# Kernel tuning notes

Measured on AMD Instinct MI355X. Metric: run time of the kernel, lower is better.

Reference implementation:

```python
import jax, jax.numpy as jnp
import numpy as np

B, NP, NT = 16, 4096, 77
QD, CD, H, DH = 512, 768, 8, 64
INNER = H * DH


def setup_inputs() -> dict:
    key = jax.random.key(0)
    ks = jax.random.split(key, 8)
    s = 0.02
    return {
        "x": jax.random.normal(ks[0], (B, NP, QD), jnp.float32),
        "context": jax.random.normal(ks[1], (B, NT, CD), jnp.float32),
        "mask": jnp.ones((B, NP, NT), jnp.int32),
        "Wq": jax.random.normal(ks[2], (QD, INNER), jnp.float32) * s,
        "Wk": jax.random.normal(ks[3], (CD, INNER), jnp.float32) * s,
        "Wv": jax.random.normal(ks[4], (CD, INNER), jnp.float32) * s,
        "Wo": jax.random.normal(ks[5], (INNER, QD), jnp.float32) * s,
        "bo": jnp.zeros((QD,), jnp.float32),
    }


def reference(x, context, mask, Wq, Wk, Wv, Wo, bo):
    scale = 1.0 / jnp.sqrt(jnp.asarray(DH, x.dtype))
    # projections -> (B, H, N, DH)
    q = (x @ Wq).reshape(B, NP, H, DH).transpose(0, 2, 1, 3)
    k = (context @ Wk).reshape(B, NT, H, DH).transpose(0, 2, 1, 3)
    v = (context @ Wv).reshape(B, NT, H, DH).transpose(0, 2, 1, 3)
    # scores (B, H, NP, NT)
    attn = jnp.einsum("bhqd,bhkd->bhqk", q, k) * scale
    attn = jnp.where(mask[:, None, :, :] == 0, -jnp.inf, attn)
    attn = jax.nn.softmax(attn, axis=-1)
    out = jnp.einsum("bhqk,bhkd->bhqd", attn, v)
    out = out.transpose(0, 2, 1, 3).reshape(B, NP, INNER)
    return out @ Wo + bo
```

## Files before the change

kernel.cpp:

```cpp
#include <hip/hip_runtime.h>


typedef _Float16 half_t;
typedef _Float16 half8 __attribute__((ext_vector_type(8)));
typedef float f32x4 __attribute__((ext_vector_type(4)));
typedef unsigned int u32;

#define NB 16
#define NP 4096
#define NT 77
#define NTP 96
#define QD 512
#define CD 768
#define NH 8
#define DH 64
#define INNER 512
#define MKV (NB * NT)

__device__ __forceinline__ void stage16(const void* g, void* l) {
    __builtin_amdgcn_global_load_lds((const __attribute__((address_space(1))) u32*)g,
                                     (__attribute__((address_space(3))) u32*)l, 16, 0, 0);
}

__device__ __forceinline__ f32x4 mfma16(half8 a, half8 b, f32x4 c) {
    return __builtin_amdgcn_mfma_f32_16x16x32_f16(a, b, c, 0, 0, 0);
}

__global__ __launch_bounds__(256) void kTrans2(const float* __restrict__ in0,
                                               const float* __restrict__ in1,
                                               half_t* __restrict__ out0,
                                               half_t* __restrict__ out1,
                                               int K, int N) {
    const float* in = blockIdx.z ? in1 : in0;
    half_t* out = blockIdx.z ? out1 : out0;
    __shared__ float tile[32][33];
    int tx = threadIdx.x & 31, ty = threadIdx.x >> 5;
    int kb = blockIdx.y * 32, nb = blockIdx.x * 32;
    for (int r = ty; r < 32; r += 8)
        tile[r][tx] = in[(size_t)(kb + r) * N + nb + tx];
    __syncthreads();
    for (int r = ty; r < 32; r += 8)
        out[(size_t)(nb + r) * K + kb + tx] = (half_t)tile[tx][r];
}

__global__ __launch_bounds__(256) void kKVproj(const float* __restrict__ Ctx,
                                               const half_t* __restrict__ WkT,
                                               const half_t* __restrict__ WvT,
                                               half_t* __restrict__ Kp,
                                               half_t* __restrict__ VTp) {
    __shared__ alignas(16) half_t As[64 * 64];
    __shared__ alignas(16) half_t Bs[128 * 64];
    const int t = threadIdx.x, w = t >> 6, lane = t & 63;
    const int c0 = lane & 15, q4 = lane >> 4;
    const int rx = c0 & 7;
    const int m0 = blockIdx.y * 64;
    const int n0g = blockIdx.x * 128;
    const int z = n0g >= 512;
    const int n0 = n0g - z * 512;
    const half_t* WT = z ? WvT : WkT;

    f32x4 acc[4][2] = {};
    for (int k0 = 0; k0 < CD; k0 += 64) {
        for (int q = 0; q < 2; ++q) {
            int c = q * 256 + t;
            int row = c >> 3, ch = c & 7;
            int gr = m0 + row; if (gr > MKV - 1) gr = MKV - 1;
            const float* src = Ctx + (size_t)gr * CD + k0 + ch * 8;
            f32x4 f0 = *(const f32x4*)src;
            f32x4 f1 = *(const f32x4*)(src + 4);
            half8 hv;
            for (int e = 0; e < 4; ++e) { hv[e] = (half_t)f0[e]; hv[4 + e] = (half_t)f1[e]; }
            *(half8*)&As[row * 64 + ((ch ^ (row & 7)) * 8)] = hv;
        }
        for (int q = 0; q < 4; ++q) {
            int c = q * 256 + t;
            int row = c >> 3, k8 = c & 7;
            stage16(WT + (size_t)(n0 + row) * CD + k0 + (k8 ^ (row & 7)) * 8, &Bs[c * 8]);
        }
        __syncthreads();
        for (int ks = 0; ks < 2; ++ks) {
            int ch = ks * 4 + q4;
            int cx = (ch ^ rx) * 8;
            half8 a[4], b[2];
            for (int i = 0; i < 4; ++i)
                a[i] = *(const half8*)&As[(16 * i + c0) * 64 + cx];
            for (int j = 0; j < 2; ++j)
                b[j] = *(const half8*)&Bs[(w * 32 + 16 * j + c0) * 64 + cx];
            for (int i = 0; i < 4; ++i)
                for (int j = 0; j < 2; ++j)
                    acc[i][j] = mfma16(a[i], b[j], acc[i][j]);
        }
        __syncthreads();
    }
    for (int i = 0; i < 4; ++i)
        for (int j = 0; j < 2; ++j)
            for (int r = 0; r < 4; ++r) {
                int row = m0 + 16 * i + q4 * 4 + r;
                if (row >= MKV) continue;
                int col = n0 + w * 32 + 16 * j + c0;
                int b = row / NT, tt = row - b * NT;
                int h = col >> 6, d = col & 63;
                half_t v = (half_t)acc[i][j][r];
                if (!z) Kp[(((size_t)b * NH + h) * NTP + tt) * DH + d] = v;
                else    VTp[(((size_t)b * NH + h) * DH + d) * NTP + tt] = v;
            }
}

__global__ __launch_bounds__(256) void kQproj(const float* __restrict__ X,
                                              const half_t* __restrict__ WqT,
                                              half_t* __restrict__ Q) {
    __shared__ alignas(16) half_t As[128 * 64];
    __shared__ alignas(16) half_t Bs[128 * 64];
    const int t = threadIdx.x, w = t >> 6, lane = t & 63;
    const int c0 = lane & 15, q4 = lane >> 4;
    const int rx = c0 & 7;
    const int wm = w & 1, wn = w >> 1;
    const int bid = blockIdx.x;
    const int wid = (bid & 7) * 256 + (bid >> 3);
    const int m0 = (wid >> 2) * 128, n0 = (wid & 3) * 128;

    f32x4 acc[4][4] = {};
    for (int k0 = 0; k0 < QD; k0 += 64) {
        for (int q = 0; q < 4; ++q) {
            int c = q * 256 + t;
            int row = c >> 3, ch = c & 7;
            const float* src = X + (size_t)(m0 + row) * QD + k0 + ch * 8;
            f32x4 f0 = *(const f32x4*)src;
            f32x4 f1 = *(const f32x4*)(src + 4);
            half8 hv;
            for (int e = 0; e < 4; ++e) { hv[e] = (half_t)f0[e]; hv[4 + e] = (half_t)f1[e]; }
            *(half8*)&As[row * 64 + ((ch ^ (row & 7)) * 8)] = hv;
        }
        for (int q = 0; q < 4; ++q) {
            int c = q * 256 + t;
            int row = c >> 3, k8 = c & 7;
            stage16(WqT + (size_t)(n0 + row) * QD + k0 + (k8 ^ (row & 7)) * 8, &Bs[c * 8]);
        }
        __syncthreads();
        for (int ks = 0; ks < 2; ++ks) {
            int cx = ((ks * 4 + q4) ^ rx) * 8;
            half8 a[4];
            for (int i = 0; i < 4; ++i)
                a[i] = *(const half8*)&As[(wm * 64 + 16 * i + c0) * 64 + cx];
            for (int j = 0; j < 4; ++j) {
                half8 bv = *(const half8*)&Bs[(wn * 64 + 16 * j + c0) * 64 + cx];
                for (int i = 0; i < 4; ++i)
                    acc[i][j] = mfma16(a[i], bv, acc[i][j]);
            }
        }
        __syncthreads();
    }
    for (int i = 0; i < 4; ++i)
        for (int j = 0; j < 4; ++j)
            for (int r = 0; r < 4; ++r) {
                int row = m0 + wm * 64 + 16 * i + q4 * 4 + r;
                int col = n0 + wn * 64 + 16 * j + c0;
                Q[(size_t)row * INNER + col] = (half_t)acc[i][j][r];
            }
}

__global__ __launch_bounds__(256) void kAttn(half_t* __restrict__ Q,
                                             const half_t* __restrict__ Kp,
                                             const half_t* __restrict__ VTp,
                                             const int* __restrict__ mask) {
    __shared__ alignas(16) half_t Qs[128 * 104];
    __shared__ alignas(16) half_t Ks[NTP * 72];
    __shared__ alignas(16) half_t VTs[DH * 104];
    const int t = threadIdx.x, w = t >> 6, lane = t & 63;
    const int c0 = lane & 15, q4 = lane >> 4;
    const int qt = blockIdx.x, h = blockIdx.y, b = blockIdx.z;
    const int q0 = qt * 128;
    const size_t qbase = ((size_t)b * NP + q0) * INNER + h * DH;

    for (int q = 0; q < 4; ++q) {
        int c = q * 256 + t, m = c >> 3, k8 = (c & 7) * 8;
        *(uint4*)&Qs[m * 104 + k8] = *(const uint4*)(Q + qbase + (size_t)m * INNER + k8);
    }
    const half_t* Kh = Kp + ((size_t)b * NH + h) * NTP * DH;
    for (int q = 0; q < 3; ++q) {
        int c = q * 256 + t, r = c >> 3, k8 = (c & 7) * 8;
        *(uint4*)&Ks[r * 72 + k8] = *(const uint4*)(Kh + r * DH + k8);
    }
    const half_t* Vh = VTp + ((size_t)b * NH + h) * DH * NTP;
    for (int q = 0; q < 3; ++q) {
        int c = q * 256 + t, r = c / 12, t8 = (c % 12) * 8;
        *(uint4*)&VTs[r * 104 + t8] = *(const uint4*)(Vh + r * NTP + t8);
    }
    __syncthreads();

    const int r0 = w * 32;
    f32x4 sacc[2][6] = {};
    for (int ks = 0; ks < 2; ++ks) {
        half8 a0 = *(const half8*)&Qs[(r0 + c0) * 104 + ks * 32 + q4 * 8];
        half8 a1 = *(const half8*)&Qs[(r0 + 16 + c0) * 104 + ks * 32 + q4 * 8];
        for (int j = 0; j < 6; ++j) {
            half8 bv = *(const half8*)&Ks[(16 * j + c0) * 72 + ks * 32 + q4 * 8];
            sacc[0][j] = mfma16(a0, bv, sacc[0][j]);
            sacc[1][j] = mfma16(a1, bv, sacc[1][j]);
        }
    }

    for (int i = 0; i < 2; ++i)
        for (int r = 0; r < 4; ++r) {
            int qrow = r0 + 16 * i + q4 * 4 + r;
            const int* mrow = mask + ((size_t)b * NP + q0 + qrow) * NT;
            float sv[6];
            for (int j = 0; j < 6; ++j) {
                int tt = 16 * j + c0;
                float s = sacc[i][j][r] * 0.125f;
                bool valid = (tt < NT) && (mrow[tt < NT ? tt : NT - 1] != 0);
                sv[j] = valid ? s : -1e30f;
            }
            float mx = sv[0];
            for (int j = 1; j < 6; ++j) mx = fmaxf(mx, sv[j]);
            for (int d = 1; d < 16; d <<= 1) mx = fmaxf(mx, __shfl_xor(mx, d));
            float pv[6], sum = 0.f;
            for (int j = 0; j < 6; ++j) { pv[j] = __expf(sv[j] - mx); sum += pv[j]; }
            for (int d = 1; d < 16; d <<= 1) sum += __shfl_xor(sum, d);
            float inv = 1.0f / sum;
            for (int j = 0; j < 6; ++j)
                Qs[qrow * 104 + 16 * j + c0] = (half_t)(pv[j] * inv);
        }

    f32x4 oacc[2][4] = {};
    for (int ks = 0; ks < 3; ++ks) {
        half8 a0 = *(const half8*)&Qs[(r0 + c0) * 104 + ks * 32 + q4 * 8];
        half8 a1 = *(const half8*)&Qs[(r0 + 16 + c0) * 104 + ks * 32 + q4 * 8];
        for (int j = 0; j < 4; ++j) {
            half8 bv = *(const half8*)&VTs[(16 * j + c0) * 104 + ks * 32 + q4 * 8];
            oacc[0][j] = mfma16(a0, bv, oacc[0][j]);
            oacc[1][j] = mfma16(a1, bv, oacc[1][j]);
        }
    }
    for (int i = 0; i < 2; ++i)
        for (int j = 0; j < 4; ++j)
            for (int r = 0; r < 4; ++r) {
                int qrow = r0 + 16 * i + q4 * 4 + r;
                int d = 16 * j + c0;
                Q[qbase + (size_t)qrow * INNER + d] = (half_t)oacc[2 > 1 ? i : i][j][r];
            }
}

__global__ __launch_bounds__(256) void kOproj(const half_t* __restrict__ AO,
                                              const half_t* __restrict__ WoT,
                                              const float* __restrict__ bo,
                                              float* __restrict__ out) {
    __shared__ alignas(16) half_t As[128 * 64];
    __shared__ alignas(16) half_t Bs[128 * 64];
    const int t = threadIdx.x, w = t >> 6, lane = t & 63;
    const int c0 = lane & 15, q4 = lane >> 4;
    const int rx = c0 & 7;
    const int wm = w & 1, wn = w >> 1;
    const int bid = blockIdx.x;
    const int wid = (bid & 7) * 256 + (bid >> 3);
    const int m0 = (wid >> 2) * 128, n0 = (wid & 3) * 128;

    float bj[4];
    for (int j = 0; j < 4; ++j) bj[j] = bo[n0 + wn * 64 + 16 * j + c0];

    f32x4 acc[4][4] = {};
    for (int k0 = 0; k0 < INNER; k0 += 64) {
        for (int q = 0; q < 4; ++q) {
            int c = q * 256 + t;
            int row = c >> 3, k8 = c & 7;
            stage16(AO + (size_t)(m0 + row) * INNER + k0 + (k8 ^ (row & 7)) * 8, &As[c * 8]);
        }
        for (int q = 0; q < 4; ++q) {
            int c = q * 256 + t;
            int row = c >> 3, k8 = c & 7;
            stage16(WoT + (size_t)(n0 + row) * INNER + k0 + (k8 ^ (row & 7)) * 8, &Bs[c * 8]);
        }
        __syncthreads();
        for (int ks = 0; ks < 2; ++ks) {
            int cx = ((ks * 4 + q4) ^ rx) * 8;
            half8 a[4];
            for (int i = 0; i < 4; ++i)
                a[i] = *(const half8*)&As[(wm * 64 + 16 * i + c0) * 64 + cx];
            for (int j = 0; j < 4; ++j) {
                half8 bv = *(const half8*)&Bs[(wn * 64 + 16 * j + c0) * 64 + cx];
                for (int i = 0; i < 4; ++i)
                    acc[i][j] = mfma16(a[i], bv, acc[i][j]);
            }
        }
        __syncthreads();
    }
    for (int i = 0; i < 4; ++i)
        for (int j = 0; j < 4; ++j)
            for (int r = 0; r < 4; ++r) {
                int row = m0 + wm * 64 + 16 * i + q4 * 4 + r;
                int col = n0 + wn * 64 + 16 * j + c0;
                out[(size_t)row * QD + col] = acc[i][j][r] + bj[j];
            }
}

extern "C" void kernel_launch(void* const* d_in, const int* in_sizes, int n_in,
                              void* d_out, int out_size, void* d_ws, size_t ws_size,
                              hipStream_t stream) {
    const float* x   = (const float*)d_in[0];
    const float* ctx = (const float*)d_in[1];
    const int*   msk = (const int*)d_in[2];
    const float* Wq  = (const float*)d_in[3];
    const float* Wk  = (const float*)d_in[4];
    const float* Wv  = (const float*)d_in[5];
    const float* Wo  = (const float*)d_in[6];
    const float* bo  = (const float*)d_in[7];
    float* out = (float*)d_out;

    half_t* Qws = (half_t*)d_ws;
    half_t* WqT = Qws + (size_t)NB * NP * INNER;
    half_t* WoT = WqT + (size_t)QD * INNER;
    half_t* WkT = WoT + (size_t)INNER * QD;
    half_t* WvT = WkT + (size_t)INNER * CD;
    half_t* Kp  = WvT + (size_t)INNER * CD;
    half_t* VTp = Kp + (size_t)NB * NH * NTP * DH;

    kTrans2<<<dim3(INNER / 32, QD / 32, 2), 256, 0, stream>>>(Wq, Wo, WqT, WoT, QD, INNER);
    kTrans2<<<dim3(INNER / 32, CD / 32, 2), 256, 0, stream>>>(Wk, Wv, WkT, WvT, CD, INNER);
    hipMemsetAsync(Kp, 0, (size_t)NB * NH * (NTP * DH + DH * NTP) * sizeof(half_t), stream);
    kKVproj<<<dim3(8, 20), 256, 0, stream>>>(ctx, WkT, WvT, Kp, VTp);
    kQproj<<<dim3(2048), 256, 0, stream>>>(x, WqT, Qws);
    kAttn<<<dim3(NP / 128, NH, NB), 256, 0, stream>>>(Qws, Kp, VTp, msk);
    kOproj<<<dim3(2048), 256, 0, stream>>>(Qws, WoT, bo, out);
}
```

Measured before the change: 407.4 us.

## Pack mask into bitmasks, vectorize GEMM epilogue stores, trim attention key tiles

A new kernel packs the int32 mask into two 64-bit ballot words per query row, so the attention kernel reads 16 bytes per row instead of 77 ints for each of the 8 heads. The Q-projection and O-projection epilogues use a quad transpose via lane shuffles so each lane writes 4 contiguous values, one vector store instead of four scalar stores. The attention score loop drops the sixth all-padding 16-key tile, whose probability columns are written as zero, and s_setprio is raised around the MFMA blocks. The changes add one extra launch and some shuffle work in exchange for less mask traffic and wider stores.

```diff
diff --git a/kernel.cpp b/kernel.cpp
--- a/kernel.cpp
+++ b/kernel.cpp
@@ -3,8 +3,10 @@
 
 typedef _Float16 half_t;
 typedef _Float16 half8 __attribute__((ext_vector_type(8)));
+typedef _Float16 half4_t __attribute__((ext_vector_type(4)));
 typedef float f32x4 __attribute__((ext_vector_type(4)));
 typedef unsigned int u32;
+typedef unsigned long long u64;
 
 #define NB 16
 #define NP 4096
@@ -24,6 +26,14 @@
 
 __device__ __forceinline__ f32x4 mfma16(half8 a, half8 b, f32x4 c) {
     return __builtin_amdgcn_mfma_f32_16x16x32_f16(a, b, c, 0, 0, 0);
+}
+
+__device__ __forceinline__ void quadT(float& v0, float& v1, float& v2, float& v3, int cq) {
+    float s, rr;
+    s = (cq & 1) ? v0 : v1; rr = __shfl_xor(s, 1); if (cq & 1) v0 = rr; else v1 = rr;
+    s = (cq & 1) ? v2 : v3; rr = __shfl_xor(s, 1); if (cq & 1) v2 = rr; else v3 = rr;
+    s = (cq & 2) ? v0 : v2; rr = __shfl_xor(s, 2); if (cq & 2) v0 = rr; else v2 = rr;
+    s = (cq & 2) ? v1 : v3; rr = __shfl_xor(s, 2); if (cq & 2) v1 = rr; else v3 = rr;
 }
 
 __global__ __launch_bounds__(256) void kTrans2(const float* __restrict__ in0,
@@ -43,6 +53,18 @@
         out[(size_t)(nb + r) * K + kb + tx] = (half_t)tile[tx][r];
 }
 
+__global__ __launch_bounds__(256) void kMaskPack(const int* __restrict__ mask,
+                                                 ulonglong2* __restrict__ mpk) {
+    int row = blockIdx.x * 4 + (threadIdx.x >> 6);
+    int lane = threadIdx.x & 63;
+    const int* mr = mask + (size_t)row * NT;
+    int v1 = mr[lane];
+    u64 lo = __ballot(v1 != 0);
+    int v2 = (lane < NT - 64) ? mr[64 + lane] : 0;
+    u64 hi = __ballot(v2 != 0);
+    if (lane == 0) { mpk[row].x = lo; mpk[row].y = hi; }
+}
+
 __global__ __launch_bounds__(256) void kKVproj(const float* __restrict__ Ctx,
                                                const half_t* __restrict__ WkT,
                                                const half_t* __restrict__ WvT,
@@ -79,8 +101,7 @@
         }
         __syncthreads();
         for (int ks = 0; ks < 2; ++ks) {
-            int ch = ks * 4 + q4;
-            int cx = (ch ^ rx) * 8;
+            int cx = ((ks * 4 + q4) ^ rx) * 8;
             half8 a[4], b[2];
             for (int i = 0; i < 4; ++i)
                 a[i] = *(const half8*)&As[(16 * i + c0) * 64 + cx];
@@ -150,19 +171,22 @@
         }
         __syncthreads();
     }
+    const int cq = c0 & 3;
     for (int i = 0; i < 4; ++i)
-        for (int j = 0; j < 4; ++j)
-            for (int r = 0; r < 4; ++r) {
-                int row = m0 + wm * 64 + 16 * i + q4 * 4 + r;
-                int col = n0 + wn * 64 + 16 * j + c0;
-                Q[(size_t)row * INNER + col] = (half_t)acc[i][j][r];
-            }
+        for (int j = 0; j < 4; ++j) {
+            float v0 = acc[i][j][0], v1 = acc[i][j][1], v2 = acc[i][j][2], v3 = acc[i][j][3];
+            quadT(v0, v1, v2, v3, cq);
+            int row = m0 + wm * 64 + 16 * i + q4 * 4 + cq;
+            int col = n0 + wn * 64 + 16 * j + (c0 & 12);
+            half4_t hv = {(half_t)v0, (half_t)v1, (half_t)v2, (half_t)v3};
+            *(half4_t*)&Q[(size_t)row * INNER + col] = hv;
+        }
 }
 
 __global__ __launch_bounds__(256) void kAttn(half_t* __restrict__ Q,
                                              const half_t* __restrict__ Kp,
                                              const half_t* __restrict__ VTp,
-                                             const int* __restrict__ mask) {
+                                             const ulonglong2* __restrict__ mpk) {
     __shared__ alignas(16) half_t Qs[128 * 104];
     __shared__ alignas(16) half_t Ks[NTP * 72];
     __shared__ alignas(16) half_t VTs[DH * 104];
@@ -189,40 +213,44 @@
     __syncthreads();
 
     const int r0 = w * 32;
-    f32x4 sacc[2][6] = {};
+    f32x4 sacc[2][5] = {};
+    __builtin_amdgcn_s_setprio(1);
     for (int ks = 0; ks < 2; ++ks) {
         half8 a0 = *(const half8*)&Qs[(r0 + c0) * 104 + ks * 32 + q4 * 8];
         half8 a1 = *(const half8*)&Qs[(r0 + 16 + c0) * 104 + ks * 32 + q4 * 8];
-        for (int j = 0; j < 6; ++j) {
+        for (int j = 0; j < 5; ++j) {
             half8 bv = *(const half8*)&Ks[(16 * j + c0) * 72 + ks * 32 + q4 * 8];
             sacc[0][j] = mfma16(a0, bv, sacc[0][j]);
             sacc[1][j] = mfma16(a1, bv, sacc[1][j]);
         }
     }
+    __builtin_amdgcn_s_setprio(0);
 
     for (int i = 0; i < 2; ++i)
         for (int r = 0; r < 4; ++r) {
             int qrow = r0 + 16 * i + q4 * 4 + r;
-            const int* mrow = mask + ((size_t)b * NP + q0 + qrow) * NT;
-            float sv[6];
-            for (int j = 0; j < 6; ++j) {
-                int tt = 16 * j + c0;
+            ulonglong2 mb = mpk[(size_t)b * NP + q0 + qrow];
+            float sv[5];
+            for (int j = 0; j < 5; ++j) {
+                u64 mwd = (j < 4) ? mb.x : mb.y;
+                int sh = (j < 4) ? (16 * j + c0) : c0;
                 float s = sacc[i][j][r] * 0.125f;
-                bool valid = (tt < NT) && (mrow[tt < NT ? tt : NT - 1] != 0);
-                sv[j] = valid ? s : -1e30f;
+                sv[j] = ((mwd >> sh) & 1ull) ? s : -1e30f;
             }
             float mx = sv[0];
-            for (int j = 1; j < 6; ++j) mx = fmaxf(mx, sv[j]);
+            for (int j = 1; j < 5; ++j) mx = fmaxf(mx, sv[j]);
             for (int d = 1; d < 16; d <<= 1) mx = fmaxf(mx, __shfl_xor(mx, d));
-            float pv[6], sum = 0.f;
-            for (int j = 0; j < 6; ++j) { pv[j] = __expf(sv[j] - mx); sum += pv[j]; }
+            float pv[5], sum = 0.f;
+            for (int j = 0; j < 5; ++j) { pv[j] = __expf(sv[j] - mx); sum += pv[j]; }
             for (int d = 1; d < 16; d <<= 1) sum += __shfl_xor(sum, d);
             float inv = 1.0f / sum;
-            for (int j = 0; j < 6; ++j)
+            for (int j = 0; j < 5; ++j)
                 Qs[qrow * 104 + 16 * j + c0] = (half_t)(pv[j] * inv);
+            Qs[qrow * 104 + 80 + c0] = (half_t)0.f;
         }
 
     f32x4 oacc[2][4] = {};
+    __builtin_amdgcn_s_setprio(1);
     for (int ks = 0; ks < 3; ++ks) {
         half8 a0 = *(const half8*)&Qs[(r0 + c0) * 104 + ks * 32 + q4 * 8];
         half8 a1 = *(const half8*)&Qs[(r0 + 16 + c0) * 104 + ks * 32 + q4 * 8];
@@ -232,12 +260,13 @@
             oacc[1][j] = mfma16(a1, bv, oacc[1][j]);
         }
     }
+    __builtin_amdgcn_s_setprio(0);
     for (int i = 0; i < 2; ++i)
         for (int j = 0; j < 4; ++j)
             for (int r = 0; r < 4; ++r) {
                 int qrow = r0 + 16 * i + q4 * 4 + r;
                 int d = 16 * j + c0;
-                Q[qbase + (size_t)qrow * INNER + d] = (half_t)oacc[2 > 1 ? i : i][j][r];
+                Q[qbase + (size_t)qrow * INNER + d] = (half_t)oacc[i][j][r];
             }
 }
 
@@ -255,8 +284,9 @@
     const int wid = (bid & 7) * 256 + (bid >> 3);
     const int m0 = (wid >> 2) * 128, n0 = (wid & 3) * 128;
 
-    float bj[4];
-    for (int j = 0; j < 4; ++j) bj[j] = bo[n0 + wn * 64 + 16 * j + c0];
+    f32x4 bq[4];
+    for (int j = 0; j < 4; ++j)
+        bq[j] = *(const f32x4*)&bo[n0 + wn * 64 + 16 * j + (c0 & 12)];
 
     f32x4 acc[4][4] = {};
     for (int k0 = 0; k0 < INNER; k0 += 64) {
@@ -284,13 +314,16 @@
         }
         __syncthreads();
     }
+    const int cq = c0 & 3;
     for (int i = 0; i < 4; ++i)
-        for (int j = 0; j < 4; ++j)
-            for (int r = 0; r < 4; ++r) {
-                int row = m0 + wm * 64 + 16 * i + q4 * 4 + r;
-                int col = n0 + wn * 64 + 16 * j + c0;
-                out[(size_t)row * QD + col] = acc[i][j][r] + bj[j];
-            }
+        for (int j = 0; j < 4; ++j) {
+            float v0 = acc[i][j][0], v1 = acc[i][j][1], v2 = acc[i][j][2], v3 = acc[i][j][3];
+            quadT(v0, v1, v2, v3, cq);
+            int row = m0 + wm * 64 + 16 * i + q4 * 4 + cq;
+            int col = n0 + wn * 64 + 16 * j + (c0 & 12);
+            f32x4 o = {v0 + bq[j][0], v1 + bq[j][1], v2 + bq[j][2], v3 + bq[j][3]};
+            *(f32x4*)&out[(size_t)row * QD + col] = o;
+        }
 }
 
 extern "C" void kernel_launch(void* const* d_in, const int* in_sizes, int n_in,
@@ -313,12 +346,14 @@
     half_t* WvT = WkT + (size_t)INNER * CD;
     half_t* Kp  = WvT + (size_t)INNER * CD;
     half_t* VTp = Kp + (size_t)NB * NH * NTP * DH;
+    ulonglong2* mpk = (ulonglong2*)(VTp + (size_t)NB * NH * DH * NTP);
 
     kTrans2<<<dim3(INNER / 32, QD / 32, 2), 256, 0, stream>>>(Wq, Wo, WqT, WoT, QD, INNER);
     kTrans2<<<dim3(INNER / 32, CD / 32, 2), 256, 0, stream>>>(Wk, Wv, WkT, WvT, CD, INNER);
+    kMaskPack<<<dim3(NB * NP / 4), 256, 0, stream>>>(msk, mpk);
     hipMemsetAsync(Kp, 0, (size_t)NB * NH * (NTP * DH + DH * NTP) * sizeof(half_t), stream);
     kKVproj<<<dim3(8, 20), 256, 0, stream>>>(ctx, WkT, WvT, Kp, VTp);
     kQproj<<<dim3(2048), 256, 0, stream>>>(x, WqT, Qws);
-    kAttn<<<dim3(NP / 128, NH, NB), 256, 0, stream>>>(Qws, Kp, VTp, msk);
+    kAttn<<<dim3(NP / 128, NH, NB), 256, 0, stream>>>(Qws, Kp, VTp, mpk);
     kOproj<<<dim3(2048), 256, 0, stream>>>(Qws, WoT, bo, out);
 }
```

After: 405.4 us. Within noise of the previous version (-0.5%).
